# Performance work log

Measured on AMD Instinct MI355X. Metric: run time of the kernel, lower is better.

## Reference

```python
import jax, jax.numpy as jnp
import numpy as np

B = 16384
DENSE_IN = 512
N_SPARSE = 26
EMB = 128
OUT_DIM = 512
NI = N_SPARSE + 1  # 27 rows in interaction matrix
DOT_OUT = NI * (NI + 1) // 2 + DENSE_IN  # 378 + 512 = 890


def setup_inputs() -> dict:
    key = jax.random.key(0)
    ks = jax.random.split(key, 6)
    dense_tensor = jax.random.normal(ks[0], (B, DENSE_IN), dtype=jnp.float32)
    sparse_tensor = jax.random.normal(ks[1], (B, N_SPARSE, EMB), dtype=jnp.float32)
    # nn.Linear(DENSE_IN, EMB): weight [EMB, DENSE_IN], bias [EMB]
    Wp = jax.random.normal(ks[2], (EMB, DENSE_IN), dtype=jnp.float32) * (1.0 / np.sqrt(DENSE_IN))
    bp = jax.random.normal(ks[3], (EMB,), dtype=jnp.float32) * 0.01
    # nn.Linear(DOT_OUT, OUT_DIM): weight [OUT_DIM, DOT_OUT], bias [OUT_DIM]
    Wo = jax.random.normal(ks[4], (OUT_DIM, DOT_OUT), dtype=jnp.float32) * (1.0 / np.sqrt(DOT_OUT))
    bo = jax.random.normal(ks[5], (OUT_DIM,), dtype=jnp.float32) * 0.01
    return {"dense_tensor": dense_tensor, "sparse_tensor": sparse_tensor,
            "Wp": Wp, "bp": bp, "Wo": Wo, "bo": bo}


def reference(dense_tensor, sparse_tensor, Wp, bp, Wo, bo):
    # Project dense feature into embedding space (dims differ in this config)
    dense_proj = dense_tensor @ Wp.T + bp                      # [B, EMB]
    T = jnp.concatenate([dense_proj[:, None, :], sparse_tensor], axis=1)  # [B, NI, EMB]
    Z = jnp.einsum('bie,bje->bij', T, T)                       # [B, NI, NI]
    li, lj = jnp.tril_indices(NI)                              # include diagonal (offset=0)
    Zflat = Z[:, li, lj]                                       # [B, NI*(NI+1)/2]
    Zflat = jnp.concatenate([dense_tensor, Zflat], axis=-1)    # [B, DOT_OUT]
    out = Zflat @ Wo.T + bo                                    # [B, OUT_DIM]
    return out
```

## Files before the change

### kernel.cpp

```cpp
#include <hip/hip_runtime.h>

#define NB    16384
#define DIN   512
#define NSP   26
#define EMBD  128
#define NOUT  512
#define NI_   27
#define NTRI  378
#define DOTK  890
#define KPAD  896

typedef __attribute__((ext_vector_type(8)))  short bf16x8;
typedef __attribute__((ext_vector_type(4)))  float f32x4;

__device__ __forceinline__ short f2bf(float f) {
    unsigned u = __builtin_bit_cast(unsigned, f);
    unsigned r = (u + 0x7FFFu + ((u >> 16) & 1u)) >> 16;
    return (short)r;
}

__device__ __forceinline__ bf16x8 cvt8(float4 a, float4 b) {
    bf16x8 r;
    r[0] = f2bf(a.x); r[1] = f2bf(a.y); r[2] = f2bf(a.z); r[3] = f2bf(a.w);
    r[4] = f2bf(b.x); r[5] = f2bf(b.y); r[6] = f2bf(b.z); r[7] = f2bf(b.w);
    return r;
}

__device__ __forceinline__ void gld_lds16(const void* g, void* l) {
    __builtin_amdgcn_global_load_lds((const __attribute__((address_space(1))) void*)g,
                                     (__attribute__((address_space(3))) void*)l,
                                     16, 0, 0);
}

#define CONV_N2  (NB * 64)
#define WOP_N2   (NOUT * (KPAD / 8))
#define WPB_N2   (EMBD * DIN / 8)
__global__ __launch_bounds__(256) void prep_all_k(const float* __restrict__ dense,
                                                  const float* __restrict__ Wo,
                                                  const float* __restrict__ Wp,
                                                  short* __restrict__ zfb,
                                                  short* __restrict__ wop,
                                                  short* __restrict__ wpb) {
    int idx = blockIdx.x * 256 + threadIdx.x;
    if (idx < CONV_N2) {
        int b = idx >> 6, c = (idx & 63) * 8;
        const float4* p = (const float4*)(dense + (size_t)b * DIN + c);
        *(bf16x8*)(zfb + (size_t)b * KPAD + c) = cvt8(p[0], p[1]);
    } else if (idx < CONV_N2 + WOP_N2) {
        int j = idx - CONV_N2;
        int o = j / (KPAD / 8), rem = j - o * (KPAD / 8);
        int k = rem * 8;
        const float* src = Wo + (size_t)o * DOTK + k;
        bf16x8 r;
#pragma unroll
        for (int t = 0; t < 8; ++t) r[t] = (k + t < DOTK) ? f2bf(src[t]) : (short)0;
        *(bf16x8*)(wop + (size_t)o * KPAD + k) = r;
    } else {
        int j = idx - CONV_N2 - WOP_N2;
        if (j < WPB_N2) {
            const float4* p = (const float4*)(Wp + (size_t)j * 8);
            *(bf16x8*)(wpb + (size_t)j * 8) = cvt8(p[0], p[1]);
        }
    }
}

template <int BM, int BN, bool OUTBF, int GXL2>
__global__ __launch_bounds__(256) void gemm_mfma(const short* __restrict__ A, int lda,
                                                 const short* __restrict__ Bm, int ldb,
                                                 const float* __restrict__ bias,
                                                 void* __restrict__ Cp, int ldc, int K) {
    constexpr int WM = BM / 2, WN = BN / 2;
    constexpr int MT = WM / 16, NT = WN / 16;
    __shared__ short As[2][BM * 64];
    __shared__ short Bs[2][BN * 64];

    const int tid = threadIdx.x;
    const int w = tid >> 6, l = tid & 63;
    const int wm = w >> 1, wn = w & 1;
    const int r0 = l & 15, q = l >> 4;

    const int nwg = (int)(gridDim.y << GXL2);
    const int bid = ((int)blockIdx.y << GXL2) | (int)blockIdx.x;
    const int swz = (bid & 7) * (nwg >> 3) + (bid >> 3);
    const int m0 = (swz >> GXL2) * BM;
    const int n0 = (swz & ((1 << GXL2) - 1)) * BN;

    const int lr = l >> 3, pseg = l & 7;

    auto stage = [&](int nb, int k0) {
#pragma unroll
        for (int i = 0; i < BM / 32; ++i) {
            int r = w * (BM / 4) + i * 8 + lr;
            int ls = pseg ^ (r & 7);
            gld_lds16(A + (size_t)(m0 + r) * lda + k0 + ls * 8,
                      (char*)&As[nb][0] + (w * (BM / 4) + i * 8) * 128);
        }
#pragma unroll
        for (int i = 0; i < BN / 32; ++i) {
            int r = w * (BN / 4) + i * 8 + lr;
            int ls = pseg ^ (r & 7);
            gld_lds16(Bm + (size_t)(n0 + r) * ldb + k0 + ls * 8,
                      (char*)&Bs[nb][0] + (w * (BN / 4) + i * 8) * 128);
        }
    };

    const f32x4 zero4 = {0.f, 0.f, 0.f, 0.f};
    f32x4 acc[MT][NT];
#pragma unroll
    for (int mi = 0; mi < MT; ++mi)
#pragma unroll
        for (int ni = 0; ni < NT; ++ni) acc[mi][ni] = zero4;

    stage(0, 0);
    __syncthreads();

    int cur = 0;
    for (int k0 = 0; k0 < K; k0 += 64) {
        if (k0 + 64 < K) stage(cur ^ 1, k0 + 64);
        const short* Ac = &As[cur][0];
        const short* Bc = &Bs[cur][0];

        __builtin_amdgcn_s_setprio(1);
#pragma unroll
        for (int h = 0; h < 2; ++h) {
            bf16x8 af[MT], bfr[NT];
#pragma unroll
            for (int mi = 0; mi < MT; ++mi) {
                int r = wm * WM + mi * 16 + r0;
                af[mi] = *(const bf16x8*)&Ac[r * 64 + ((h * 4 + q) ^ (r & 7)) * 8];
            }
#pragma unroll
            for (int ni = 0; ni < NT; ++ni) {
                int r = wn * WN + ni * 16 + r0;
                bfr[ni] = *(const bf16x8*)&Bc[r * 64 + ((h * 4 + q) ^ (r & 7)) * 8];
            }
#pragma unroll
            for (int mi = 0; mi < MT; ++mi)
#pragma unroll
                for (int ni = 0; ni < NT; ++ni)
                    acc[mi][ni] = __builtin_amdgcn_mfma_f32_16x16x32_bf16(
                        af[mi], bfr[ni], acc[mi][ni], 0, 0, 0);
        }
        __builtin_amdgcn_s_setprio(0);

        __syncthreads();
        cur ^= 1;
    }

#pragma unroll
    for (int mi = 0; mi < MT; ++mi) {
#pragma unroll
        for (int ni = 0; ni < NT; ++ni) {
            int col = n0 + wn * WN + ni * 16 + r0;
            float bb = bias[col];
#pragma unroll
            for (int r = 0; r < 4; ++r) {
                int row = m0 + wm * WM + mi * 16 + q * 4 + r;
                float v = acc[mi][ni][r] + bb;
                if (OUTBF) ((short*)Cp)[(size_t)row * ldc + col] = f2bf(v);
                else       ((float*)Cp)[(size_t)row * ldc + col] = v;
            }
        }
    }
}

__global__ __launch_bounds__(256) void interact_mfma(const float* __restrict__ sparse,
                                                     const short* __restrict__ dprojb,
                                                     short* __restrict__ zfb) {
    __shared__ short zt[4][384];
    const int w = threadIdx.x >> 6, l = threadIdx.x & 63;
    const int b = blockIdx.x * 4 + w;
    const int r0 = l & 15, q = l >> 4;

    const float* srow = sparse + (size_t)b * (NSP * EMBD);
    const short* dp = dprojb + (size_t)b * EMBD;

    const f32x4 zero4 = {0.f, 0.f, 0.f, 0.f};
    f32x4 acc00 = zero4, acc10 = zero4, acc11 = zero4;

#pragma unroll
    for (int kc = 0; kc < 4; ++kc) {
        int k = kc * 32 + q * 8;
        bf16x8 f0, f1;
        if (r0 == 0) {
            f0 = *(const bf16x8*)(dp + k);
        } else {
            const float* p = srow + (size_t)(r0 - 1) * EMBD + k;
            f0 = cvt8(*(const float4*)p, *(const float4*)(p + 4));
        }
        if (r0 <= 10) {
            const float* p = srow + (size_t)(15 + r0) * EMBD + k;
            f1 = cvt8(*(const float4*)p, *(const float4*)(p + 4));
        } else {
            f1 = (bf16x8){0, 0, 0, 0, 0, 0, 0, 0};
        }
        acc00 = __builtin_amdgcn_mfma_f32_16x16x32_bf16(f0, f0, acc00, 0, 0, 0);
        acc10 = __builtin_amdgcn_mfma_f32_16x16x32_bf16(f1, f0, acc10, 0, 0, 0);
        acc11 = __builtin_amdgcn_mfma_f32_16x16x32_bf16(f1, f1, acc11, 0, 0, 0);
    }

#pragma unroll
    for (int r = 0; r < 4; ++r) {
        int row, col;
        row = q * 4 + r;       col = r0;
        if (col <= row)             zt[w][row * (row + 1) / 2 + col] = f2bf(acc00[r]);
        row = 16 + q * 4 + r;  col = r0;
        if (row < NI_)              zt[w][row * (row + 1) / 2 + col] = f2bf(acc10[r]);
               col = 16 + r0;
        if (row < NI_ && col <= row) zt[w][row * (row + 1) / 2 + col] = f2bf(acc11[r]);
    }
    if (l < 6) zt[w][NTRI + l] = 0;
    const int* zrow = (const int*)zt[w];
    int* dst = (int*)(zfb + (size_t)b * KPAD + DIN);
#pragma unroll
    for (int t = 0; t < 3; ++t) dst[t * 64 + l] = zrow[t * 64 + l];
}

extern "C" void kernel_launch(void* const* d_in, const int* in_sizes, int n_in,
                              void* d_out, int out_size, void* d_ws, size_t ws_size,
                              hipStream_t stream) {
    const float* dense  = (const float*)d_in[0];
    const float* sparse = (const float*)d_in[1];
    const float* Wp     = (const float*)d_in[2];
    const float* bp     = (const float*)d_in[3];
    const float* Wo     = (const float*)d_in[4];
    const float* bo     = (const float*)d_in[5];
    float* out = (float*)d_out;

    short* zfb    = (short*)d_ws;
    short* dprojb = zfb + (size_t)NB * KPAD;
    short* wop    = dprojb + (size_t)NB * EMBD;
    short* wpb    = wop + (size_t)NOUT * KPAD;

    prep_all_k<<<(CONV_N2 + WOP_N2 + WPB_N2 + 255) / 256, 256, 0, stream>>>(
        dense, Wo, Wp, zfb, wop, wpb);

    gemm_mfma<64, 64, true, 1><<<dim3(EMBD / 64, NB / 64), 256, 0, stream>>>(
        zfb, KPAD, wpb, DIN, bp, dprojb, EMBD, DIN);

    interact_mfma<<<NB / 4, 256, 0, stream>>>(sparse, dprojb, zfb);

    gemm_mfma<128, 128, false, 2><<<dim3(NOUT / 128, NB / 128), 256, 0, stream>>>(
        zfb, KPAD, wop, KPAD, bo, out, NOUT, KPAD);
}
```

Baseline: 370.2 us.

## Fuse dense fp32-to-bf16 conversion into the dense projection GEMM

Dense-input conversion moves out of the prep kernel and into a new GEMM kernel. That kernel reads fp32 dense rows, converts them to bf16 in registers, writes them to the Z buffer and to LDS, and runs MFMA against the bf16 Wp. Each workgroup covers 32 rows across all 128 output columns, so dense is read once and the separate bf16 round trip of dense before GEMM1 is gone. The cost is smaller M tiles and register-staged A loads in place of direct LDS loads, which could lower GEMM efficiency.

Result: no change. 373.4 us (+0.9%).

```diff
diff --git a/kernel.cpp b/kernel.cpp
--- a/kernel.cpp
+++ b/kernel.cpp
@@ -32,23 +32,15 @@
                                      16, 0, 0);
 }
 
-#define CONV_N2  (NB * 64)
 #define WOP_N2   (NOUT * (KPAD / 8))
 #define WPB_N2   (EMBD * DIN / 8)
-__global__ __launch_bounds__(256) void prep_all_k(const float* __restrict__ dense,
-                                                  const float* __restrict__ Wo,
-                                                  const float* __restrict__ Wp,
-                                                  short* __restrict__ zfb,
-                                                  short* __restrict__ wop,
-                                                  short* __restrict__ wpb) {
+__global__ __launch_bounds__(256) void prep_w_k(const float* __restrict__ Wo,
+                                                const float* __restrict__ Wp,
+                                                short* __restrict__ wop,
+                                                short* __restrict__ wpb) {
     int idx = blockIdx.x * 256 + threadIdx.x;
-    if (idx < CONV_N2) {
-        int b = idx >> 6, c = (idx & 63) * 8;
-        const float4* p = (const float4*)(dense + (size_t)b * DIN + c);
-        *(bf16x8*)(zfb + (size_t)b * KPAD + c) = cvt8(p[0], p[1]);
-    } else if (idx < CONV_N2 + WOP_N2) {
-        int j = idx - CONV_N2;
-        int o = j / (KPAD / 8), rem = j - o * (KPAD / 8);
+    if (idx < WOP_N2) {
+        int o = idx / (KPAD / 8), rem = idx - o * (KPAD / 8);
         int k = rem * 8;
         const float* src = Wo + (size_t)o * DOTK + k;
         bf16x8 r;
@@ -56,10 +48,119 @@
         for (int t = 0; t < 8; ++t) r[t] = (k + t < DOTK) ? f2bf(src[t]) : (short)0;
         *(bf16x8*)(wop + (size_t)o * KPAD + k) = r;
     } else {
-        int j = idx - CONV_N2 - WOP_N2;
+        int j = idx - WOP_N2;
         if (j < WPB_N2) {
             const float4* p = (const float4*)(Wp + (size_t)j * 8);
             *(bf16x8*)(wpb + (size_t)j * 8) = cvt8(p[0], p[1]);
+        }
+    }
+}
+
+__global__ __launch_bounds__(256) void gemm1_fused(const float* __restrict__ dense,
+                                                   const short* __restrict__ wpb,
+                                                   const float* __restrict__ bp,
+                                                   short* __restrict__ zfb,
+                                                   short* __restrict__ dprojb) {
+    __shared__ short As[2][32 * 64];
+    __shared__ short Bs[2][128 * 64];
+
+    const int tid = threadIdx.x;
+    const int w = tid >> 6, l = tid & 63;
+    const int r0 = l & 15, q = l >> 4;
+
+    const int nwg = (int)gridDim.x;
+    const int bid = (int)blockIdx.x;
+    const int swz = (bid & 7) * (nwg >> 3) + (bid >> 3);
+    const int m0 = swz * 32;
+
+    const int ar = tid >> 3, ag = tid & 7;
+    const float* aptr = dense + (size_t)(m0 + ar) * DIN + ag * 8;
+    short* zptr = zfb + (size_t)(m0 + ar) * KPAD + ag * 8;
+    const int aoff = ar * 64 + (ag ^ (ar & 7)) * 8;
+
+    const int lr = l >> 3, pseg = l & 7;
+
+    auto stageB = [&](int nb, int k0) {
+#pragma unroll
+        for (int i = 0; i < 4; ++i) {
+            int r = w * 32 + i * 8 + lr;
+            int ls = pseg ^ (r & 7);
+            gld_lds16(wpb + (size_t)r * DIN + k0 + ls * 8,
+                      (char*)&Bs[nb][0] + (w * 32 + i * 8) * 128);
+        }
+    };
+
+    const f32x4 zero4 = {0.f, 0.f, 0.f, 0.f};
+    f32x4 acc[2][2];
+#pragma unroll
+    for (int mi = 0; mi < 2; ++mi)
+#pragma unroll
+        for (int ni = 0; ni < 2; ++ni) acc[mi][ni] = zero4;
+
+    stageB(0, 0);
+    {
+        float4 a0 = *(const float4*)(aptr);
+        float4 a1 = *(const float4*)(aptr + 4);
+        bf16x8 av = cvt8(a0, a1);
+        *(bf16x8*)&As[0][aoff] = av;
+        *(bf16x8*)zptr = av;
+    }
+    __syncthreads();
+
+    int cur = 0;
+    for (int k = 0; k < 8; ++k) {
+        const int k0 = k * 64;
+        const bool pf = (k < 7);
+        float4 n0, n1;
+        if (pf) {
+            stageB(cur ^ 1, k0 + 64);
+            n0 = *(const float4*)(aptr + k0 + 64);
+            n1 = *(const float4*)(aptr + k0 + 68);
+        }
+
+        __builtin_amdgcn_s_setprio(1);
+#pragma unroll
+        for (int h = 0; h < 2; ++h) {
+            bf16x8 af[2], bfr[2];
+#pragma unroll
+            for (int mi = 0; mi < 2; ++mi) {
+                int r = mi * 16 + r0;
+                af[mi] = *(const bf16x8*)&As[cur][r * 64 + ((h * 4 + q) ^ (r & 7)) * 8];
+            }
+#pragma unroll
+            for (int ni = 0; ni < 2; ++ni) {
+                int r = w * 32 + ni * 16 + r0;
+                bfr[ni] = *(const bf16x8*)&Bs[cur][r * 64 + ((h * 4 + q) ^ (r & 7)) * 8];
+            }
+#pragma unroll
+            for (int mi = 0; mi < 2; ++mi)
+#pragma unroll
+                for (int ni = 0; ni < 2; ++ni)
+                    acc[mi][ni] = __builtin_amdgcn_mfma_f32_16x16x32_bf16(
+                        af[mi], bfr[ni], acc[mi][ni], 0, 0, 0);
+        }
+        __builtin_amdgcn_s_setprio(0);
+
+        if (pf) {
+            bf16x8 av = cvt8(n0, n1);
+            *(bf16x8*)&As[cur ^ 1][aoff] = av;
+            *(bf16x8*)(zptr + k0 + 64) = av;
+        }
+        __syncthreads();
+        cur ^= 1;
+    }
+
+#pragma unroll
+    for (int mi = 0; mi < 2; ++mi) {
+#pragma unroll
+        for (int ni = 0; ni < 2; ++ni) {
+            int col = w * 32 + ni * 16 + r0;
+            float bb = bp[col];
+#pragma unroll
+            for (int r = 0; r < 4; ++r) {
+                int row = m0 + mi * 16 + q * 4 + r;
+                dprojb[(size_t)row * EMBD + col] = f2bf(acc[mi][ni][r] + bb);
+            }
         }
     }
 }
@@ -232,11 +333,9 @@
     short* wop    = dprojb + (size_t)NB * EMBD;
     short* wpb    = wop + (size_t)NOUT * KPAD;
 
-    prep_all_k<<<(CONV_N2 + WOP_N2 + WPB_N2 + 255) / 256, 256, 0, stream>>>(
-        dense, Wo, Wp, zfb, wop, wpb);
-
-    gemm_mfma<64, 64, true, 1><<<dim3(EMBD / 64, NB / 64), 256, 0, stream>>>(
-        zfb, KPAD, wpb, DIN, bp, dprojb, EMBD, DIN);
+    prep_w_k<<<(WOP_N2 + WPB_N2) / 256, 256, 0, stream>>>(Wo, Wp, wop, wpb);
+
+    gemm1_fused<<<NB / 32, 256, 0, stream>>>(dense, wpb, bp, zfb, dprojb);
 
     interact_mfma<<<NB / 4, 256, 0, stream>>>(sparse, dprojb, zfb);
 
```
